# Kernel optimization log

Measured on AMD Instinct MI355X. Metric: run time of the kernel, lower is better.

The kernel has to match this reference:

```python
import jax, jax.numpy as jnp
import numpy as np

B, N, IN_DIM, DIM, KNN = 8, 2048, 128, 128, 16
POS_H = 64
ATTN_H = DIM * 4
EPS = 1e-5
SCALE = 1.0 / np.sqrt(DIM).astype(np.float32)


def setup_inputs() -> dict:
    key = jax.random.key(0)
    ks = jax.random.split(key, 10)
    nrm = lambda k, shape, s=0.02: jax.random.normal(k, shape, jnp.float32) * s
    return dict(
        ori_x=jax.random.normal(ks[0], (B, N, IN_DIM), jnp.float32),
        pos=jax.random.normal(ks[1], (B, N, 3), jnp.float32),
        w_in=nrm(ks[2], (IN_DIM, DIM)),
        w_qkv=nrm(ks[3], (DIM, 3 * DIM)),
        w_out=nrm(ks[4], (DIM, IN_DIM)),
        pos_w1=nrm(ks[5], (3, POS_H)), pos_b1=jnp.zeros((POS_H,), jnp.float32),
        pos_bn_g=jnp.ones((POS_H,), jnp.float32), pos_bn_b=jnp.zeros((POS_H,), jnp.float32),
        pos_bn_m=jnp.zeros((POS_H,), jnp.float32), pos_bn_v=jnp.ones((POS_H,), jnp.float32),
        pos_w2=nrm(ks[6], (POS_H, DIM)), pos_b2=jnp.zeros((DIM,), jnp.float32),
        attn_w1=nrm(ks[7], (DIM, ATTN_H)), attn_b1=jnp.zeros((ATTN_H,), jnp.float32),
        attn_bn_g=jnp.ones((ATTN_H,), jnp.float32), attn_bn_b=jnp.zeros((ATTN_H,), jnp.float32),
        attn_bn_m=jnp.zeros((ATTN_H,), jnp.float32), attn_bn_v=jnp.ones((ATTN_H,), jnp.float32),
        attn_w2=nrm(ks[8], (ATTN_H, DIM)), attn_b2=jnp.zeros((DIM,), jnp.float32),
    )


def _bn_eval(x, g, b, m, v):
    # BatchNorm2d in eval mode; channel is the last axis in our [b,n,k,C] layout
    return (x - m) * (g * jax.lax.rsqrt(v + EPS)) + b


def reference(ori_x, pos, w_in, w_qkv, w_out,
              pos_w1, pos_b1, pos_bn_g, pos_bn_b, pos_bn_m, pos_bn_v, pos_w2, pos_b2,
              attn_w1, attn_b1, attn_bn_g, attn_bn_b, attn_bn_m, attn_bn_v, attn_w2, attn_b2):
    x = ori_x @ w_in                                  # [b,n,dim]
    qkv = x @ w_qkv
    q, k, v = jnp.split(qkv, 3, axis=-1)              # each [b,n,dim]

    # pairwise squared distances [b,n,n] (monotone in rel_dist -> same topk)
    sq = jnp.sum(pos * pos, axis=-1)
    d2 = sq[:, :, None] + sq[:, None, :] - 2.0 * jnp.einsum('bnd,bmd->bnm', pos, pos)
    _, idx = jax.lax.top_k(-d2, KNN)                  # [b,n,KNN] nearest neighbors

    gather = jax.vmap(lambda t, i: t[i])              # [n,C],[n,k] -> [n,k,C] per batch
    k_g = gather(k, idx)                              # [b,n,k,dim]
    v_g = gather(v, idx)
    pos_g = gather(pos, idx)                          # [b,n,k,3]

    rel_pos = pos[:, :, None, :] - pos_g              # [b,n,k,3]
    pe = jax.nn.relu(_bn_eval(rel_pos @ pos_w1 + pos_b1, pos_bn_g, pos_bn_b, pos_bn_m, pos_bn_v))
    pe = pe @ pos_w2 + pos_b2                         # [b,n,k,dim]

    qk_rel = q[:, :, None, :] - k_g                   # [b,n,k,dim]
    h = jax.nn.relu(_bn_eval((qk_rel + pe) @ attn_w1 + attn_b1,
                             attn_bn_g, attn_bn_b, attn_bn_m, attn_bn_v))
    h = h @ attn_w2 + attn_b2                         # [b,n,k,dim]

    attn = jax.nn.softmax(h * SCALE, axis=-2)         # softmax over neighbors
    agg = jnp.sum(attn * (v_g + pe), axis=2)          # [b,n,dim]
    return agg @ w_out + ori_x
```

## Files before the change

kernel.cpp:

```cpp
#include <hip/hip_runtime.h>

#define EPS 1e-5f

constexpr int NB   = 8;
constexpr int NN   = 2048;
constexpr int DIM  = 128;
constexpr int KNN  = 16;
constexpr int AH   = 512;
constexpr int NPTS = NB * NN;
constexpr float SCALE = 0.08838834764831845f;

typedef __attribute__((ext_vector_type(8))) short short8;
typedef __attribute__((ext_vector_type(4))) float floatx4;

__device__ __forceinline__ short f2bf(float f) {
  union { float f; unsigned u; } a; a.f = f;
  return (short)((a.u + 0x8000u) >> 16);
}
__device__ __forceinline__ float bf2f(short s) {
  union { unsigned u; float f; } a; a.u = ((unsigned)(unsigned short)s) << 16;
  return a.f;
}

__global__ __launch_bounds__(256) void gemm_f32(
    const float* __restrict__ A, const float* __restrict__ W,
    float* __restrict__ C, int M, int N, int K)
{
  __shared__ float As[64][33];
  __shared__ float Ws[32][65];
  const int bm = blockIdx.x * 64, bn = blockIdx.y * 64;
  const int tid = threadIdx.x;
  const int tx = tid & 15, ty = tid >> 4;
  float acc[4][4] = {};
  for (int k0 = 0; k0 < K; k0 += 32) {
#pragma unroll
    for (int i = 0; i < 8; ++i) {
      int e = tid + i * 256;
      As[e >> 5][e & 31] = A[(size_t)(bm + (e >> 5)) * K + k0 + (e & 31)];
    }
#pragma unroll
    for (int i = 0; i < 8; ++i) {
      int e = tid + i * 256;
      Ws[e >> 6][e & 63] = W[(size_t)(k0 + (e >> 6)) * N + bn + (e & 63)];
    }
    __syncthreads();
#pragma unroll
    for (int kk = 0; kk < 32; ++kk) {
      float a[4], w[4];
#pragma unroll
      for (int i = 0; i < 4; ++i) a[i] = As[ty * 4 + i][kk];
#pragma unroll
      for (int j = 0; j < 4; ++j) w[j] = Ws[kk][tx * 4 + j];
#pragma unroll
      for (int i = 0; i < 4; ++i)
#pragma unroll
        for (int j = 0; j < 4; ++j)
          acc[i][j] += a[i] * w[j];
    }
    __syncthreads();
  }
#pragma unroll
  for (int i = 0; i < 4; ++i)
#pragma unroll
    for (int j = 0; j < 4; ++j)
      C[(size_t)(bm + ty * 4 + i) * N + bn + tx * 4 + j] = acc[i][j];
}

__global__ __launch_bounds__(256) void knn_kernel(
    const float* __restrict__ pos_t, int* __restrict__ idx_out)
{
  const int tid = threadIdx.x;
  const int lane = tid & 63;
  const int p = blockIdx.x * 4 + (tid >> 6);
  const int b = p >> 11, i = p & (NN - 1);
  const float* px = pos_t + (size_t)b * 3 * NN;
  const float* py = px + NN;
  const float* pz = py + NN;
  const float xi = px[i], yi = py[i], zi = pz[i];
  const float sqi = xi * xi + yi * yi + zi * zi;
  float v[32];
#pragma unroll
  for (int t = 0; t < 32; ++t) {
    int j = t * 64 + lane;
    float xj = px[j], yj = py[j], zj = pz[j];
    float sqj = xj * xj + yj * yj + zj * zj;
    float dot = xi * xj + yi * yj + zi * zj;
    v[t] = sqi + sqj - 2.0f * dot;
  }
  for (int s = 0; s < KNN; ++s) {
    float bv = 3.4e38f; int bj = 1 << 30;
#pragma unroll
    for (int t = 0; t < 32; ++t) {
      if (v[t] < bv) { bv = v[t]; bj = t * 64 + lane; }
    }
#pragma unroll
    for (int m = 1; m < 64; m <<= 1) {
      float ov = __shfl_xor(bv, m);
      int   oj = __shfl_xor(bj, m);
      if (ov < bv || (ov == bv && oj < bj)) { bv = ov; bj = oj; }
    }
    if (lane == 0) idx_out[(size_t)p * KNN + s] = bj;
#pragma unroll
    for (int t = 0; t < 32; ++t)
      if (bj == t * 64 + lane) v[t] = 3.4e38f;
  }
}

__global__ __launch_bounds__(256) void pack_weights(
    const float* __restrict__ attn_w1, const float* __restrict__ attn_w2,
    const float* __restrict__ pos_w2, const float* __restrict__ Wf,
    const float* __restrict__ w_out, const float* __restrict__ pos,
    const float* __restrict__ attn_b1, const float* __restrict__ abn_g,
    const float* __restrict__ abn_b, const float* __restrict__ abn_m,
    const float* __restrict__ abn_v,
    const float* __restrict__ pos_b1, const float* __restrict__ pbn_g,
    const float* __restrict__ pbn_b, const float* __restrict__ pbn_m,
    const float* __restrict__ pbn_v, const float* __restrict__ pos_b2,
    short* __restrict__ w1p, short* __restrict__ w2p, short* __restrict__ pw2p,
    short* __restrict__ wfp, short* __restrict__ wop,
    float* __restrict__ biasq,
    float* __restrict__ t1sc, float* __restrict__ t1bi,
    float* __restrict__ phsc, float* __restrict__ phbi,
    float* __restrict__ pos_t)
{
  int t = blockIdx.x * 256 + threadIdx.x;
  if (t < 65536) {
    int j = t & 7, lane = (t >> 3) & 63, ks = (t >> 9) & 3, nt = (t >> 11) & 3, ch = t >> 13;
    int q = lane >> 4, cc = lane & 15;
    int k = ks * 32 + q * 8 + j, n = ch * 64 + nt * 16 + cc;
    w1p[t] = f2bf(attn_w1[(size_t)k * AH + n]);
  } else if (t < 131072) {
    int e = t - 65536;
    int j = e & 7, lane = (e >> 3) & 63, ks = (e >> 9) & 1, nt = (e >> 10) & 7, ch = e >> 13;
    int q = lane >> 4, cc = lane & 15;
    int k = ch * 64 + ks * 32 + q * 8 + j, n = nt * 16 + cc;
    w2p[e] = f2bf(attn_w2[(size_t)k * DIM + n]);
  } else if (t < 139264) {
    int e = t - 131072;
    int j = e & 7, lane = (e >> 3) & 63, ks = (e >> 9) & 1, nt = e >> 10;
    int q = lane >> 4, cc = lane & 15;
    int k = ks * 32 + q * 8 + j, n = nt * 16 + cc;
    pw2p[e] = f2bf(pos_w2[(size_t)k * DIM + n]);
  } else if (t < 188416) {
    int e = t - 139264;
    int j = e & 7, lane = (e >> 3) & 63, ks = (e >> 9) & 3, nt = (e >> 11) & 7, nc = e >> 14;
    int q = lane >> 4, cc = lane & 15;
    int k = ks * 32 + q * 8 + j, n = nc * 128 + nt * 16 + cc;
    wfp[e] = f2bf(Wf[(size_t)k * 384 + n]);
  } else if (t < 204800) {
    int e = t - 188416;
    int j = e & 7, lane = (e >> 3) & 63, ks = (e >> 9) & 3, nt = (e >> 11) & 7;
    int q = lane >> 4, cc = lane & 15;
    int k = ks * 32 + q * 8 + j, n = nt * 16 + cc;
    wop[e] = f2bf(w_out[(size_t)k * DIM + n]);
  } else if (t < 205184) {
    int c = t - 204800;
    biasq[c] = (c < 128) ? pos_b2[c] : ((c < 256) ? 0.0f : pos_b2[c - 256]);
  } else if (t < 205696) {
    int c = t - 205184;
    t1sc[c] = abn_g[c] * rsqrtf(abn_v[c] + EPS);
  } else if (t < 206208) {
    int c = t - 205696;
    float sc = abn_g[c] * rsqrtf(abn_v[c] + EPS);
    t1bi[c] = (attn_b1[c] - abn_m[c]) * sc + abn_b[c];
  } else if (t < 206272) {
    int c = t - 206208;
    phsc[c] = pbn_g[c] * rsqrtf(pbn_v[c] + EPS);
  } else if (t < 206336) {
    int c = t - 206272;
    float sc = pbn_g[c] * rsqrtf(pbn_v[c] + EPS);
    phbi[c] = (pos_b1[c] - pbn_m[c]) * sc + pbn_b[c];
  } else if (t < 206336 + NPTS * 3) {
    int e = t - 206336;
    int p = e / 3, d = e - p * 3;
    int b = p >> 11, n = p & (NN - 1);
    pos_t[((size_t)b * 3 + d) * NN + n] = pos[e];
  }
}

__global__ __launch_bounds__(256, 4) void gemm_in(
    const float* __restrict__ A, const short* __restrict__ wfp,
    const float* __restrict__ biasq, short* __restrict__ C)
{
  __shared__ short As[64 * 128];
  const int tid = threadIdx.x;
  const int lane = tid & 63, w = tid >> 6;
  const int wr = w >> 1, wc = w & 1;
  const int q = lane >> 4, cc = lane & 15;
  const int row0 = blockIdx.x * 64;
#pragma unroll
  for (int it = 0; it < 4; ++it) {
    int e = tid + it * 256;
    int row = e >> 4, cg = e & 15;
    const float* src = A + (size_t)(row0 + row) * 128 + cg * 8;
    float4 f0 = *(const float4*)src, f1 = *(const float4*)(src + 4);
    short8 v;
    v[0] = f2bf(f0.x); v[1] = f2bf(f0.y); v[2] = f2bf(f0.z); v[3] = f2bf(f0.w);
    v[4] = f2bf(f1.x); v[5] = f2bf(f1.y); v[6] = f2bf(f1.z); v[7] = f2bf(f1.w);
    *(short8*)(As + row * 128 + ((cg ^ (row & 15)) << 3)) = v;
  }
  __syncthreads();
  for (int nc = 0; nc < 3; ++nc) {
    floatx4 acc[2][4];
#pragma unroll
    for (int i = 0; i < 2; ++i)
#pragma unroll
      for (int jt = 0; jt < 4; ++jt) acc[i][jt] = (floatx4){0.f, 0.f, 0.f, 0.f};
#pragma unroll
    for (int ks = 0; ks < 4; ++ks) {
      short8 a8[2], b8[4];
#pragma unroll
      for (int i = 0; i < 2; ++i) {
        int row = (wr * 2 + i) * 16 + cc;
        a8[i] = *(const short8*)(As + row * 128 + (((ks * 4 + q) ^ cc) << 3));
      }
#pragma unroll
      for (int jt = 0; jt < 4; ++jt)
        b8[jt] = *(const short8*)(wfp + ((((nc * 8 + wc * 4 + jt) * 4 + ks) * 64 + lane) << 3));
#pragma unroll
      for (int i = 0; i < 2; ++i)
#pragma unroll
        for (int jt = 0; jt < 4; ++jt)
          acc[i][jt] = __builtin_amdgcn_mfma_f32_16x16x32_bf16(a8[i], b8[jt], acc[i][jt], 0, 0, 0);
    }
#pragma unroll
    for (int jt = 0; jt < 4; ++jt) {
      int colG = nc * 128 + (wc * 4 + jt) * 16 + cc;
      float bv = biasq[colG];
#pragma unroll
      for (int i = 0; i < 2; ++i)
#pragma unroll
        for (int r = 0; r < 4; ++r) {
          int row = (wr * 2 + i) * 16 + q * 4 + r;
          C[(size_t)(row0 + row) * 384 + colG] = f2bf(acc[i][jt][r] + bv);
        }
    }
  }
}

__global__ __launch_bounds__(256, 4) void gemm_out(
    const float* __restrict__ A, const short* __restrict__ wop,
    const float* __restrict__ R, float* __restrict__ C)
{
  __shared__ short As[64 * 128];
  const int tid = threadIdx.x;
  const int lane = tid & 63, w = tid >> 6;
  const int wr = w >> 1, wc = w & 1;
  const int q = lane >> 4, cc = lane & 15;
  const int row0 = blockIdx.x * 64;
#pragma unroll
  for (int it = 0; it < 4; ++it) {
    int e = tid + it * 256;
    int row = e >> 4, cg = e & 15;
    const float* src = A + (size_t)(row0 + row) * 128 + cg * 8;
    float4 f0 = *(const float4*)src, f1 = *(const float4*)(src + 4);
    short8 v;
    v[0] = f2bf(f0.x); v[1] = f2bf(f0.y); v[2] = f2bf(f0.z); v[3] = f2bf(f0.w);
    v[4] = f2bf(f1.x); v[5] = f2bf(f1.y); v[6] = f2bf(f1.z); v[7] = f2bf(f1.w);
    *(short8*)(As + row * 128 + ((cg ^ (row & 15)) << 3)) = v;
  }
  __syncthreads();
  floatx4 acc[2][4];
#pragma unroll
  for (int i = 0; i < 2; ++i)
#pragma unroll
    for (int jt = 0; jt < 4; ++jt) acc[i][jt] = (floatx4){0.f, 0.f, 0.f, 0.f};
#pragma unroll
  for (int ks = 0; ks < 4; ++ks) {
    short8 a8[2], b8[4];
#pragma unroll
    for (int i = 0; i < 2; ++i) {
      int row = (wr * 2 + i) * 16 + cc;
      a8[i] = *(const short8*)(As + row * 128 + (((ks * 4 + q) ^ cc) << 3));
    }
#pragma unroll
    for (int jt = 0; jt < 4; ++jt)
      b8[jt] = *(const short8*)(wop + ((((wc * 4 + jt) * 4 + ks) * 64 + lane) << 3));
#pragma unroll
    for (int i = 0; i < 2; ++i)
#pragma unroll
      for (int jt = 0; jt < 4; ++jt)
        acc[i][jt] = __builtin_amdgcn_mfma_f32_16x16x32_bf16(a8[i], b8[jt], acc[i][jt], 0, 0, 0);
  }
#pragma unroll
  for (int jt = 0; jt < 4; ++jt) {
    int col = (wc * 4 + jt) * 16 + cc;
#pragma unroll
    for (int i = 0; i < 2; ++i)
#pragma unroll
      for (int r = 0; r < 4; ++r) {
        int row = (wr * 2 + i) * 16 + q * 4 + r;
        size_t o = (size_t)(row0 + row) * 128 + col;
        C[o] = acc[i][jt][r] + R[o];
      }
  }
}

__global__ __launch_bounds__(256, 3) void fused_attn(
    const float* __restrict__ pos, const short* __restrict__ qkv,
    const int* __restrict__ knn_idx,
    const float* __restrict__ pos_w1,
    const short* __restrict__ w1p, const short* __restrict__ w2p,
    const short* __restrict__ pw2p,
    const float* __restrict__ t1sc, const float* __restrict__ t1bi,
    const float* __restrict__ phsc, const float* __restrict__ phbi,
    const float* __restrict__ attn_b2,
    float* __restrict__ agg)
{
  __shared__ short a_s[64 * 128];
  __shared__ short vpe_s[64 * 128];
  __shared__ short t1_s[2][64 * 64];
  __shared__ short q_ss[4 * 128];
  __shared__ float relp_s[64 * 4];
  __shared__ int   nbr_s[64];

  const int tid = threadIdx.x;
  const int lane = tid & 63, w = tid >> 6;
  const int wr = w >> 1, wc = w & 1;
  const int q = lane >> 4, cc = lane & 15;
  const int bb = blockIdx.x & 7;
  const int gp0 = bb * NN + (blockIdx.x >> 3) * 4;

  if (tid < 64) nbr_s[tid] = knn_idx[(size_t)gp0 * KNN + tid];
  if (tid >= 64 && tid < 128) {
    int e = tid - 64;
    int p = e >> 4, seg = e & 15;
    *(short8*)(q_ss + p * 128 + seg * 8) =
        *(const short8*)(qkv + (size_t)(gp0 + p) * 384 + seg * 8);
  }
  __syncthreads();
  if (tid < 64) {
    int p = tid >> 4;
    int j = nbr_s[tid];
    const float* pa = pos + (size_t)(gp0 + p) * 3;
    const float* pj = pos + ((size_t)bb * NN + j) * 3;
    relp_s[tid * 4 + 0] = pa[0] - pj[0];
    relp_s[tid * 4 + 1] = pa[1] - pj[1];
    relp_s[tid * 4 + 2] = pa[2] - pj[2];
  }
  __syncthreads();

#pragma unroll
  for (int r2 = 0; r2 < 16; ++r2) {
    int e = tid + r2 * 256;
    int row = e >> 6, c = e & 63;
    float lin = relp_s[row * 4] * pos_w1[c] + relp_s[row * 4 + 1] * pos_w1[64 + c]
              + relp_s[row * 4 + 2] * pos_w1[128 + c];
    t1_s[0][row * 64 + (((c >> 3) ^ (row & 7)) << 3) + (c & 7)] =
        f2bf(fmaxf(lin * phsc[c] + phbi[c], 0.0f));
  }
  __syncthreads();

  floatx4 pe[2][4];
#pragma unroll
  for (int i = 0; i < 2; ++i)
#pragma unroll
    for (int jt = 0; jt < 4; ++jt) pe[i][jt] = (floatx4){0.f, 0.f, 0.f, 0.f};
#pragma unroll
  for (int ks = 0; ks < 2; ++ks) {
    short8 a8[2];
#pragma unroll
    for (int i = 0; i < 2; ++i) {
      int row = (wr * 2 + i) * 16 + cc;
      a8[i] = *(const short8*)(t1_s[0] + row * 64 + (((ks * 4 + q) ^ (row & 7)) << 3));
    }
#pragma unroll
    for (int jt = 0; jt < 4; ++jt) {
      short8 b8 = *(const short8*)(pw2p + ((((wc * 4 + jt) * 2 + ks) * 64 + lane) << 3));
#pragma unroll
      for (int i = 0; i < 2; ++i)
        pe[i][jt] = __builtin_amdgcn_mfma_f32_16x16x32_bf16(a8[i], b8, pe[i][jt], 0, 0, 0);
    }
  }

#pragma unroll
  for (int i = 0; i < 2; ++i) {
    int rt = wr * 2 + i;
#pragma unroll
    for (int jt = 0; jt < 4; ++jt) {
      int col = (wc * 4 + jt) * 16 + cc;
      float qv = bf2f(q_ss[rt * 128 + col]);
#pragma unroll
      for (int r = 0; r < 4; ++r) {
        int row = rt * 16 + q * 4 + r;
        const short* kv = qkv + ((size_t)bb * NN + nbr_s[row]) * 384;
        float pev = pe[i][jt][r];
        int slot = row * 128 + (((col >> 3) ^ (row & 15)) << 3) + (col & 7);
        a_s[slot]   = f2bf(qv - bf2f(kv[128 + col]) + pev);
        vpe_s[slot] = f2bf(bf2f(kv[256 + col]) + pev);
      }
    }
  }
  __syncthreads();

  floatx4 hacc[2][4];
#pragma unroll
  for (int i = 0; i < 2; ++i)
#pragma unroll
    for (int jt = 0; jt < 4; ++jt) hacc[i][jt] = (floatx4){0.f, 0.f, 0.f, 0.f};

  for (int ch = 0; ch < 8; ++ch) {
    short* t1b = t1_s[ch & 1];
    floatx4 tacc[2][2];
#pragma unroll
    for (int i = 0; i < 2; ++i)
#pragma unroll
      for (int jt = 0; jt < 2; ++jt) tacc[i][jt] = (floatx4){0.f, 0.f, 0.f, 0.f};
#pragma unroll
    for (int ks = 0; ks < 4; ++ks) {
      short8 a8[2], b8[2];
#pragma unroll
      for (int i = 0; i < 2; ++i) {
        int row = (wr * 2 + i) * 16 + cc;
        a8[i] = *(const short8*)(a_s + row * 128 + (((ks * 4 + q) ^ cc) << 3));
      }
#pragma unroll
      for (int jt = 0; jt < 2; ++jt)
        b8[jt] = *(const short8*)(w1p + ((((ch * 4 + wc * 2 + jt) * 4 + ks) * 64 + lane) << 3));
#pragma unroll
      for (int i = 0; i < 2; ++i)
#pragma unroll
        for (int jt = 0; jt < 2; ++jt)
          tacc[i][jt] = __builtin_amdgcn_mfma_f32_16x16x32_bf16(a8[i], b8[jt], tacc[i][jt], 0, 0, 0);
    }
#pragma unroll
    for (int jt = 0; jt < 2; ++jt) {
      int colL = (wc * 2 + jt) * 16 + cc;
      int colG = ch * 64 + colL;
      float sc = t1sc[colG], bi = t1bi[colG];
#pragma unroll
      for (int i = 0; i < 2; ++i)
#pragma unroll
        for (int r = 0; r < 4; ++r) {
          int row = (wr * 2 + i) * 16 + q * 4 + r;
          t1b[row * 64 + (((colL >> 3) ^ (row & 7)) << 3) + (colL & 7)] =
              f2bf(fmaxf(tacc[i][jt][r] * sc + bi, 0.0f));
        }
    }
    __syncthreads();
#pragma unroll
    for (int ks = 0; ks < 2; ++ks) {
      short8 a8[2], b8[4];
#pragma unroll
      for (int i = 0; i < 2; ++i) {
        int row = (wr * 2 + i) * 16 + cc;
        a8[i] = *(const short8*)(t1b + row * 64 + (((ks * 4 + q) ^ (row & 7)) << 3));
      }
#pragma unroll
      for (int jt = 0; jt < 4; ++jt)
        b8[jt] = *(const short8*)(w2p + ((((ch * 8 + wc * 4 + jt) * 2 + ks) * 64 + lane) << 3));
#pragma unroll
      for (int i = 0; i < 2; ++i)
#pragma unroll
        for (int jt = 0; jt < 4; ++jt)
          hacc[i][jt] = __builtin_amdgcn_mfma_f32_16x16x32_bf16(a8[i], b8[jt], hacc[i][jt], 0, 0, 0);
    }
  }

#pragma unroll
  for (int i = 0; i < 2; ++i) {
    int rt = wr * 2 + i;
#pragma unroll
    for (int jt = 0; jt < 4; ++jt) {
      int col = (wc * 4 + jt) * 16 + cc;
      float b2v = attn_b2[col];
      float v0[4], mx = -3.4e38f;
#pragma unroll
      for (int r = 0; r < 4; ++r) {
        v0[r] = (hacc[i][jt][r] + b2v) * SCALE;
        mx = fmaxf(mx, v0[r]);
      }
      mx = fmaxf(mx, __shfl_xor(mx, 16));
      mx = fmaxf(mx, __shfl_xor(mx, 32));
      float ex[4], sum = 0.f;
#pragma unroll
      for (int r = 0; r < 4; ++r) { ex[r] = __expf(v0[r] - mx); sum += ex[r]; }
      sum += __shfl_xor(sum, 16);
      sum += __shfl_xor(sum, 32);
      float inv = 1.0f / sum;
      float part = 0.f;
#pragma unroll
      for (int r = 0; r < 4; ++r) {
        int row = rt * 16 + q * 4 + r;
        int slot = row * 128 + (((col >> 3) ^ (row & 15)) << 3) + (col & 7);
        part += ex[r] * bf2f(vpe_s[slot]);
      }
      part += __shfl_xor(part, 16);
      part += __shfl_xor(part, 32);
      if (q == 0) agg[(size_t)(gp0 + rt) * DIM + col] = part * inv;
    }
  }
}

extern "C" void kernel_launch(void* const* d_in, const int* in_sizes, int n_in,
                              void* d_out, int out_size, void* d_ws, size_t ws_size,
                              hipStream_t stream)
{
  const float* ori_x    = (const float*)d_in[0];
  const float* pos      = (const float*)d_in[1];
  const float* w_in     = (const float*)d_in[2];
  const float* w_qkv    = (const float*)d_in[3];
  const float* w_out    = (const float*)d_in[4];
  const float* pos_w1   = (const float*)d_in[5];
  const float* pos_b1   = (const float*)d_in[6];
  const float* pos_bn_g = (const float*)d_in[7];
  const float* pos_bn_b = (const float*)d_in[8];
  const float* pos_bn_m = (const float*)d_in[9];
  const float* pos_bn_v = (const float*)d_in[10];
  const float* pos_w2   = (const float*)d_in[11];
  const float* pos_b2   = (const float*)d_in[12];
  const float* attn_w1  = (const float*)d_in[13];
  const float* attn_b1  = (const float*)d_in[14];
  const float* attn_bn_g = (const float*)d_in[15];
  const float* attn_bn_b = (const float*)d_in[16];
  const float* attn_bn_m = (const float*)d_in[17];
  const float* attn_bn_v = (const float*)d_in[18];
  const float* attn_w2  = (const float*)d_in[19];
  const float* attn_b2  = (const float*)d_in[20];
  float* out = (float*)d_out;

  float* agg  = (float*)d_ws;
  float* Wf   = agg;
  short* qkvb = (short*)(agg + (size_t)NPTS * DIM);
  int*   idx  = (int*)(qkvb + (size_t)NPTS * 3 * DIM);
  short* w1p  = (short*)(idx + (size_t)NPTS * KNN);
  short* w2p  = w1p + 65536;
  short* pw2p = w2p + 65536;
  short* wfp  = pw2p + 8192;
  short* wop  = wfp + 49152;
  float* biasq = (float*)(wop + 16384);
  float* t1sc = biasq + 384;
  float* t1bi = t1sc + 512;
  float* phsc = t1bi + 512;
  float* phbi = phsc + 64;
  float* pos_t = phbi + 64;

  gemm_f32<<<dim3(2, 6), 256, 0, stream>>>(w_in, w_qkv, Wf, 128, 384, 128);
  pack_weights<<<998, 256, 0, stream>>>(attn_w1, attn_w2, pos_w2, Wf, w_out, pos,
      attn_b1, attn_bn_g, attn_bn_b, attn_bn_m, attn_bn_v,
      pos_b1, pos_bn_g, pos_bn_b, pos_bn_m, pos_bn_v, pos_b2,
      w1p, w2p, pw2p, wfp, wop, biasq, t1sc, t1bi, phsc, phbi, pos_t);
  gemm_in<<<NPTS / 64, 256, 0, stream>>>(ori_x, wfp, biasq, qkvb);
  knn_kernel<<<NPTS / 4, 256, 0, stream>>>(pos_t, idx);
  fused_attn<<<NPTS / 4, 256, 0, stream>>>(pos, qkvb, idx, pos_w1,
      w1p, w2p, pw2p, t1sc, t1bi, phsc, phbi, attn_b2, agg);
  gemm_out<<<NPTS / 64, 256, 0, stream>>>(agg, wop, ori_x, out);
}
```

Measured before the change: 360.7 us.

## Fuse kNN search and output projection into attention kernel, fold weight GEMM into packing

Each attention block now runs the brute-force kNN search for its four points itself, one per wave, and writes the neighbour indices straight to shared memory. The block also applies the output projection with MFMA on a zero-padded 16-row tile and adds the residual, so the separate knn, gemm_out and small weight-product kernels disappear along with their global round-trips for idx and agg. The w_in@w_qkv product is now computed inline per element in pack_weights. In exchange, the output GEMM wastes 12 of 16 MFMA rows, kNN register pressure now sits inside the heavy attention kernel and can lower occupancy, and agg is rounded to bf16 before projection.

```diff
diff --git a/kernel.cpp b/kernel.cpp
--- a/kernel.cpp
+++ b/kernel.cpp
@@ -22,93 +22,10 @@
   return a.f;
 }
 
-__global__ __launch_bounds__(256) void gemm_f32(
-    const float* __restrict__ A, const float* __restrict__ W,
-    float* __restrict__ C, int M, int N, int K)
-{
-  __shared__ float As[64][33];
-  __shared__ float Ws[32][65];
-  const int bm = blockIdx.x * 64, bn = blockIdx.y * 64;
-  const int tid = threadIdx.x;
-  const int tx = tid & 15, ty = tid >> 4;
-  float acc[4][4] = {};
-  for (int k0 = 0; k0 < K; k0 += 32) {
-#pragma unroll
-    for (int i = 0; i < 8; ++i) {
-      int e = tid + i * 256;
-      As[e >> 5][e & 31] = A[(size_t)(bm + (e >> 5)) * K + k0 + (e & 31)];
-    }
-#pragma unroll
-    for (int i = 0; i < 8; ++i) {
-      int e = tid + i * 256;
-      Ws[e >> 6][e & 63] = W[(size_t)(k0 + (e >> 6)) * N + bn + (e & 63)];
-    }
-    __syncthreads();
-#pragma unroll
-    for (int kk = 0; kk < 32; ++kk) {
-      float a[4], w[4];
-#pragma unroll
-      for (int i = 0; i < 4; ++i) a[i] = As[ty * 4 + i][kk];
-#pragma unroll
-      for (int j = 0; j < 4; ++j) w[j] = Ws[kk][tx * 4 + j];
-#pragma unroll
-      for (int i = 0; i < 4; ++i)
-#pragma unroll
-        for (int j = 0; j < 4; ++j)
-          acc[i][j] += a[i] * w[j];
-    }
-    __syncthreads();
-  }
-#pragma unroll
-  for (int i = 0; i < 4; ++i)
-#pragma unroll
-    for (int j = 0; j < 4; ++j)
-      C[(size_t)(bm + ty * 4 + i) * N + bn + tx * 4 + j] = acc[i][j];
-}
-
-__global__ __launch_bounds__(256) void knn_kernel(
-    const float* __restrict__ pos_t, int* __restrict__ idx_out)
-{
-  const int tid = threadIdx.x;
-  const int lane = tid & 63;
-  const int p = blockIdx.x * 4 + (tid >> 6);
-  const int b = p >> 11, i = p & (NN - 1);
-  const float* px = pos_t + (size_t)b * 3 * NN;
-  const float* py = px + NN;
-  const float* pz = py + NN;
-  const float xi = px[i], yi = py[i], zi = pz[i];
-  const float sqi = xi * xi + yi * yi + zi * zi;
-  float v[32];
-#pragma unroll
-  for (int t = 0; t < 32; ++t) {
-    int j = t * 64 + lane;
-    float xj = px[j], yj = py[j], zj = pz[j];
-    float sqj = xj * xj + yj * yj + zj * zj;
-    float dot = xi * xj + yi * yj + zi * zj;
-    v[t] = sqi + sqj - 2.0f * dot;
-  }
-  for (int s = 0; s < KNN; ++s) {
-    float bv = 3.4e38f; int bj = 1 << 30;
-#pragma unroll
-    for (int t = 0; t < 32; ++t) {
-      if (v[t] < bv) { bv = v[t]; bj = t * 64 + lane; }
-    }
-#pragma unroll
-    for (int m = 1; m < 64; m <<= 1) {
-      float ov = __shfl_xor(bv, m);
-      int   oj = __shfl_xor(bj, m);
-      if (ov < bv || (ov == bv && oj < bj)) { bv = ov; bj = oj; }
-    }
-    if (lane == 0) idx_out[(size_t)p * KNN + s] = bj;
-#pragma unroll
-    for (int t = 0; t < 32; ++t)
-      if (bj == t * 64 + lane) v[t] = 3.4e38f;
-  }
-}
-
 __global__ __launch_bounds__(256) void pack_weights(
     const float* __restrict__ attn_w1, const float* __restrict__ attn_w2,
-    const float* __restrict__ pos_w2, const float* __restrict__ Wf,
+    const float* __restrict__ pos_w2, const float* __restrict__ w_in,
+    const float* __restrict__ w_qkv,
     const float* __restrict__ w_out, const float* __restrict__ pos,
     const float* __restrict__ attn_b1, const float* __restrict__ abn_g,
     const float* __restrict__ abn_b, const float* __restrict__ abn_m,
@@ -146,7 +63,11 @@
     int j = e & 7, lane = (e >> 3) & 63, ks = (e >> 9) & 3, nt = (e >> 11) & 7, nc = e >> 14;
     int q = lane >> 4, cc = lane & 15;
     int k = ks * 32 + q * 8 + j, n = nc * 128 + nt * 16 + cc;
-    wfp[e] = f2bf(Wf[(size_t)k * 384 + n]);
+    float s = 0.0f;
+#pragma unroll 8
+    for (int m = 0; m < 128; ++m)
+      s += w_in[(size_t)k * DIM + m] * w_qkv[(size_t)m * 384 + n];
+    wfp[e] = f2bf(s);
   } else if (t < 204800) {
     int e = t - 188416;
     int j = e & 7, lane = (e >> 3) & 63, ks = (e >> 9) & 3, nt = (e >> 11) & 7;
@@ -238,74 +159,15 @@
   }
 }
 
-__global__ __launch_bounds__(256, 4) void gemm_out(
-    const float* __restrict__ A, const short* __restrict__ wop,
-    const float* __restrict__ R, float* __restrict__ C)
-{
-  __shared__ short As[64 * 128];
-  const int tid = threadIdx.x;
-  const int lane = tid & 63, w = tid >> 6;
-  const int wr = w >> 1, wc = w & 1;
-  const int q = lane >> 4, cc = lane & 15;
-  const int row0 = blockIdx.x * 64;
-#pragma unroll
-  for (int it = 0; it < 4; ++it) {
-    int e = tid + it * 256;
-    int row = e >> 4, cg = e & 15;
-    const float* src = A + (size_t)(row0 + row) * 128 + cg * 8;
-    float4 f0 = *(const float4*)src, f1 = *(const float4*)(src + 4);
-    short8 v;
-    v[0] = f2bf(f0.x); v[1] = f2bf(f0.y); v[2] = f2bf(f0.z); v[3] = f2bf(f0.w);
-    v[4] = f2bf(f1.x); v[5] = f2bf(f1.y); v[6] = f2bf(f1.z); v[7] = f2bf(f1.w);
-    *(short8*)(As + row * 128 + ((cg ^ (row & 15)) << 3)) = v;
-  }
-  __syncthreads();
-  floatx4 acc[2][4];
-#pragma unroll
-  for (int i = 0; i < 2; ++i)
-#pragma unroll
-    for (int jt = 0; jt < 4; ++jt) acc[i][jt] = (floatx4){0.f, 0.f, 0.f, 0.f};
-#pragma unroll
-  for (int ks = 0; ks < 4; ++ks) {
-    short8 a8[2], b8[4];
-#pragma unroll
-    for (int i = 0; i < 2; ++i) {
-      int row = (wr * 2 + i) * 16 + cc;
-      a8[i] = *(const short8*)(As + row * 128 + (((ks * 4 + q) ^ cc) << 3));
-    }
-#pragma unroll
-    for (int jt = 0; jt < 4; ++jt)
-      b8[jt] = *(const short8*)(wop + ((((wc * 4 + jt) * 4 + ks) * 64 + lane) << 3));
-#pragma unroll
-    for (int i = 0; i < 2; ++i)
-#pragma unroll
-      for (int jt = 0; jt < 4; ++jt)
-        acc[i][jt] = __builtin_amdgcn_mfma_f32_16x16x32_bf16(a8[i], b8[jt], acc[i][jt], 0, 0, 0);
-  }
-#pragma unroll
-  for (int jt = 0; jt < 4; ++jt) {
-    int col = (wc * 4 + jt) * 16 + cc;
-#pragma unroll
-    for (int i = 0; i < 2; ++i)
-#pragma unroll
-      for (int r = 0; r < 4; ++r) {
-        int row = (wr * 2 + i) * 16 + q * 4 + r;
-        size_t o = (size_t)(row0 + row) * 128 + col;
-        C[o] = acc[i][jt][r] + R[o];
-      }
-  }
-}
-
 __global__ __launch_bounds__(256, 3) void fused_attn(
-    const float* __restrict__ pos, const short* __restrict__ qkv,
-    const int* __restrict__ knn_idx,
+    const float* __restrict__ pos_t, const short* __restrict__ qkv,
     const float* __restrict__ pos_w1,
     const short* __restrict__ w1p, const short* __restrict__ w2p,
-    const short* __restrict__ pw2p,
+    const short* __restrict__ pw2p, const short* __restrict__ wop,
     const float* __restrict__ t1sc, const float* __restrict__ t1bi,
     const float* __restrict__ phsc, const float* __restrict__ phbi,
     const float* __restrict__ attn_b2,
-    float* __restrict__ agg)
+    const float* __restrict__ ori_x, float* __restrict__ out)
 {
   __shared__ short a_s[64 * 128];
   __shared__ short vpe_s[64 * 128];
@@ -319,24 +181,57 @@
   const int wr = w >> 1, wc = w & 1;
   const int q = lane >> 4, cc = lane & 15;
   const int bb = blockIdx.x & 7;
-  const int gp0 = bb * NN + (blockIdx.x >> 3) * 4;
-
-  if (tid < 64) nbr_s[tid] = knn_idx[(size_t)gp0 * KNN + tid];
-  if (tid >= 64 && tid < 128) {
+  const int base = (blockIdx.x >> 3) * 4;
+  const int gp0 = bb * NN + base;
+
+  const float* px = pos_t + (size_t)bb * 3 * NN;
+  const float* py = px + NN;
+  const float* pz = py + NN;
+
+  {
+    const int il = base + w;
+    const float xi = px[il], yi = py[il], zi = pz[il];
+    const float sqi = xi * xi + yi * yi + zi * zi;
+    float v[32];
+#pragma unroll
+    for (int t = 0; t < 32; ++t) {
+      int j = t * 64 + lane;
+      float xj = px[j], yj = py[j], zj = pz[j];
+      float sqj = xj * xj + yj * yj + zj * zj;
+      float dot = xi * xj + yi * yj + zi * zj;
+      v[t] = sqi + sqj - 2.0f * dot;
+    }
+    for (int s = 0; s < KNN; ++s) {
+      float bv = 3.4e38f; int bj = 1 << 30;
+#pragma unroll
+      for (int t = 0; t < 32; ++t) {
+        if (v[t] < bv) { bv = v[t]; bj = t * 64 + lane; }
+      }
+#pragma unroll
+      for (int m = 1; m < 64; m <<= 1) {
+        float ov = __shfl_xor(bv, m);
+        int   oj = __shfl_xor(bj, m);
+        if (ov < bv || (ov == bv && oj < bj)) { bv = ov; bj = oj; }
+      }
+      if (lane == 0) nbr_s[w * KNN + s] = bj;
+#pragma unroll
+      for (int t = 0; t < 32; ++t)
+        if (bj == t * 64 + lane) v[t] = 3.4e38f;
+    }
+  }
+  __syncthreads();
+
+  if (tid < 64) {
+    int p = tid >> 4;
+    int j = nbr_s[tid];
+    relp_s[tid * 4 + 0] = px[base + p] - px[j];
+    relp_s[tid * 4 + 1] = py[base + p] - py[j];
+    relp_s[tid * 4 + 2] = pz[base + p] - pz[j];
+  } else if (tid < 128) {
     int e = tid - 64;
     int p = e >> 4, seg = e & 15;
     *(short8*)(q_ss + p * 128 + seg * 8) =
         *(const short8*)(qkv + (size_t)(gp0 + p) * 384 + seg * 8);
-  }
-  __syncthreads();
-  if (tid < 64) {
-    int p = tid >> 4;
-    int j = nbr_s[tid];
-    const float* pa = pos + (size_t)(gp0 + p) * 3;
-    const float* pj = pos + ((size_t)bb * NN + j) * 3;
-    relp_s[tid * 4 + 0] = pa[0] - pj[0];
-    relp_s[tid * 4 + 1] = pa[1] - pj[1];
-    relp_s[tid * 4 + 2] = pa[2] - pj[2];
   }
   __syncthreads();
 
@@ -457,6 +352,12 @@
     }
   }
 
+  short* agg_s = t1_s[0];
+#pragma unroll
+  for (int r2 = 0; r2 < 6; ++r2) {
+    int e = tid + r2 * 256;
+    agg_s[(4 + (e >> 7)) * 128 + (e & 127)] = 0;
+  }
 #pragma unroll
   for (int i = 0; i < 2; ++i) {
     int rt = wr * 2 + i;
@@ -487,7 +388,34 @@
       }
       part += __shfl_xor(part, 16);
       part += __shfl_xor(part, 32);
-      if (q == 0) agg[(size_t)(gp0 + rt) * DIM + col] = part * inv;
+      if (q == 0) agg_s[rt * 128 + col] = f2bf(part * inv);
+    }
+  }
+  __syncthreads();
+
+  {
+    floatx4 oacc[2];
+#pragma unroll
+    for (int jt = 0; jt < 2; ++jt) oacc[jt] = (floatx4){0.f, 0.f, 0.f, 0.f};
+#pragma unroll
+    for (int ks = 0; ks < 4; ++ks) {
+      short8 a8 = *(const short8*)(agg_s + cc * 128 + ks * 32 + q * 8);
+#pragma unroll
+      for (int jt = 0; jt < 2; ++jt) {
+        short8 b8 = *(const short8*)(wop + ((((w * 2 + jt) * 4 + ks) * 64 + lane) << 3));
+        oacc[jt] = __builtin_amdgcn_mfma_f32_16x16x32_bf16(a8, b8, oacc[jt], 0, 0, 0);
+      }
+    }
+    if (q == 0) {
+#pragma unroll
+      for (int jt = 0; jt < 2; ++jt) {
+        int col = (w * 2 + jt) * 16 + cc;
+#pragma unroll
+        for (int r = 0; r < 4; ++r) {
+          size_t o = (size_t)(gp0 + r) * 128 + col;
+          out[o] = oacc[jt][r] + ori_x[o];
+        }
+      }
     }
   }
 }
@@ -519,11 +447,8 @@
   const float* attn_b2  = (const float*)d_in[20];
   float* out = (float*)d_out;
 
-  float* agg  = (float*)d_ws;
-  float* Wf   = agg;
-  short* qkvb = (short*)(agg + (size_t)NPTS * DIM);
-  int*   idx  = (int*)(qkvb + (size_t)NPTS * 3 * DIM);
-  short* w1p  = (short*)(idx + (size_t)NPTS * KNN);
+  short* qkvb = (short*)d_ws;
+  short* w1p  = qkvb + (size_t)NPTS * 3 * DIM;
   short* w2p  = w1p + 65536;
   short* pw2p = w2p + 65536;
   short* wfp  = pw2p + 8192;
@@ -535,14 +460,12 @@
   float* phbi = phsc + 64;
   float* pos_t = phbi + 64;
 
-  gemm_f32<<<dim3(2, 6), 256, 0, stream>>>(w_in, w_qkv, Wf, 128, 384, 128);
-  pack_weights<<<998, 256, 0, stream>>>(attn_w1, attn_w2, pos_w2, Wf, w_out, pos,
+  pack_weights<<<998, 256, 0, stream>>>(attn_w1, attn_w2, pos_w2, w_in, w_qkv,
+      w_out, pos,
       attn_b1, attn_bn_g, attn_bn_b, attn_bn_m, attn_bn_v,
       pos_b1, pos_bn_g, pos_bn_b, pos_bn_m, pos_bn_v, pos_b2,
       w1p, w2p, pw2p, wfp, wop, biasq, t1sc, t1bi, phsc, phbi, pos_t);
   gemm_in<<<NPTS / 64, 256, 0, stream>>>(ori_x, wfp, biasq, qkvb);
-  knn_kernel<<<NPTS / 4, 256, 0, stream>>>(pos_t, idx);
-  fused_attn<<<NPTS / 4, 256, 0, stream>>>(pos, qkvb, idx, pos_w1,
-      w1p, w2p, pw2p, t1sc, t1bi, phsc, phbi, attn_b2, agg);
-  gemm_out<<<NPTS / 64, 256, 0, stream>>>(agg, wop, ori_x, out);
-}
+  fused_attn<<<NPTS / 4, 256, 0, stream>>>(pos_t, qkvb, pos_w1,
+      w1p, w2p, pw2p, wop, t1sc, t1bi, phsc, phbi, attn_b2, ori_x, out);
+}
```

Measured after the change: 369.8 us. 1.03x slower.
